# Optimization experiments

Measured on AMD Instinct MI355X. Metric: run time of the kernel, lower is better.

Reference implementation:

```python
import jax, jax.numpy as jnp
import numpy as np

H_S = 4
W_S = 4


def setup_inputs() -> dict:
    key = jax.random.key(0)
    k1, k2 = jax.random.split(key)
    x1 = jax.random.normal(k1, (8, 128, 96, 320), dtype=jnp.float32)
    x2 = jax.random.normal(k2, (8, 128, 96, 320), dtype=jnp.float32)
    return {"x1": x1, "x2": x2}


def reference(x1, x2):
    # torch F.pad p2d=(h_s,h_s,w_s,w_s) pads last dim (W) by h_s and H by w_s
    b, c, h, w = x1.shape
    padded = jnp.pad(x2, ((0, 0), (0, 0), (W_S, W_S), (H_S, H_S)))
    costs = []
    for y in range(2 * H_S + 1):
        for x in range(2 * W_S + 1):
            sl = padded[:, :, y:y + h, x:x + w]  # [B,C,H,W]
            costs.append(jnp.mean(x1 * sl, axis=1))  # [B,H,W]
    cost_vol = jnp.stack(costs, axis=1)  # [B,81,H,W]
    return jax.nn.leaky_relu(cost_vol, negative_slope=0.1)
```

## Files before the change

### kernel.cpp

```cpp
#include <hip/hip_runtime.h>
#include <stdint.h>


#define CCH   128
#define HH    96
#define WW    320
#define HWs   (HH * WW)
#define CHWs  (CCH * HWs)
#define ND    81

#define TH 4
#define WT 32
#define SW 40
#define SR 12
#define KC 32
#define KP 40
#define OP 132

typedef __attribute__((ext_vector_type(8))) short        short8;
typedef __attribute__((ext_vector_type(4))) float        floatx4;
typedef __attribute__((ext_vector_type(4))) unsigned int uint4v;

__device__ __forceinline__ unsigned int bf16rne(float f) {
  unsigned int u = __float_as_uint(f);
  return (u + 0x7fffu + ((u >> 16) & 1u)) >> 16;
}
__device__ __forceinline__ unsigned int pk2(float lo, float hi) {
  return bf16rne(lo) | (bf16rne(hi) << 16);
}

__global__ __launch_bounds__(512, 4) void cost_volume_kernel(
    const float* __restrict__ x1g, const float* __restrict__ x2g,
    float* __restrict__ out)
{
  extern __shared__ char smem[];
  short* x2s  = (short*)smem;
  float* obuf = (float*)smem;

  const int b  = blockIdx.x & 7;
  const int g  = blockIdx.x >> 3;
  const int hs = g % 24;
  const int ws = g / 24;
  const int h0 = hs * TH;
  const int W0 = ws * WT;

  const int t    = threadIdx.x;
  const int wave = t >> 6;
  const int lane = t & 63;
  const int hl   = wave >> 1;
  const int mt   = wave & 1;
  const int q    = lane >> 4;
  const int ln   = lane & 15;

  const float* x1b = x1g + (size_t)b * CHWs;
  const float* x2b = x2g + (size_t)b * CHWs;

  int x2_go[4], x2_lo[4];
#pragma unroll
  for (int s = 0; s < 4; ++s) {
    int u = t + s * 512;
    if (u < SR * SW * 4) {
      int j  = u % SW;
      int ro = u / SW;
      int o  = ro & 3;
      int r  = ro >> 2;
      int gr = h0 - 4 + r;
      int gc = W0 - 4 + j;
      x2_lo[s] = (r * SW + j) * KP + o * 8;
      x2_go[s] = (gr >= 0 && gr < HH && gc >= 0 && gc < WW)
                   ? (o * 8 * HWs + gr * WW + gc) : -1;
    } else { x2_lo[s] = -1; x2_go[s] = -1; }
  }
  const int x1off = (h0 + hl) * WW + W0 + mt * 16 + ln;

  floatx4 acc[9][2] = {};

  for (int kc = 0; kc < CCH / KC; ++kc) {
    const int cbase = kc * KC * HWs;

    const float* p1 = x1b + cbase + (size_t)q * 8 * HWs + x1off;
    float a0 = p1[0 * HWs], a1 = p1[1 * HWs], a2 = p1[2 * HWs], a3 = p1[3 * HWs];
    float a4 = p1[4 * HWs], a5 = p1[5 * HWs], a6 = p1[6 * HWs], a7 = p1[7 * HWs];

#pragma unroll
    for (int s = 0; s < 4; ++s) {
      if (x2_lo[s] >= 0) {
        unsigned int p01 = 0, p23 = 0, p45 = 0, p67 = 0;
        if (x2_go[s] >= 0) {
          const float* p = x2b + cbase + x2_go[s];
          float f0 = p[0 * HWs], f1 = p[1 * HWs], f2 = p[2 * HWs], f3 = p[3 * HWs];
          float f4 = p[4 * HWs], f5 = p[5 * HWs], f6 = p[6 * HWs], f7 = p[7 * HWs];
          p01 = pk2(f0, f1); p23 = pk2(f2, f3);
          p45 = pk2(f4, f5); p67 = pk2(f6, f7);
        }
        *(uint4v*)&x2s[x2_lo[s]] = (uint4v){p01, p23, p45, p67};
      }
    }

    short8 af;
    {
      uint4v av = (uint4v){pk2(a0, a1), pk2(a2, a3), pk2(a4, a5), pk2(a6, a7)};
      af = *(short8*)&av;
    }
    __syncthreads();

#pragma unroll
    for (int dyi = 0; dyi < 9; ++dyi) {
      const int r = hl + dyi;
#pragma unroll
      for (int jn = 0; jn < 2; ++jn) {
        int jc = (mt + jn) * 16 + ln;
        if (jc > SW - 1) jc = SW - 1;
        const short8 bf = *(const short8*)&x2s[(r * SW + jc) * KP + q * 8];
        acc[dyi][jn] = __builtin_amdgcn_mfma_f32_16x16x32_bf16(af, bf, acc[dyi][jn], 0, 0, 0);
      }
    }
    __syncthreads();
  }

  const size_t obase = (size_t)b * (ND * (size_t)HWs);
#pragma unroll
  for (int ph = 0; ph < 2; ++ph) {
    const int d0 = ph ? 5 : 0, d1 = ph ? 9 : 5;
#pragma unroll
    for (int dyi = 0; dyi < 9; ++dyi) {
      if (dyi < d0 || dyi >= d1) continue;
#pragma unroll
      for (int jn = 0; jn < 2; ++jn)
#pragma unroll
        for (int reg = 0; reg < 4; ++reg) {
          const int m   = q * 4 + reg;
          const int dxi = jn * 16 + ln - m;
          if (dxi >= 0 && dxi < 9) {
            float v = acc[dyi][jn][reg] * (1.0f / 128.0f);
            v = (v < 0.0f) ? 0.1f * v : v;
            obuf[((dyi - d0) * 9 + dxi) * OP + hl * WT + mt * 16 + m] = v;
          }
        }
    }
    __syncthreads();
    const int nd   = (d1 - d0) * 9;
    const int dbas = d0 * 9;
    for (int idx = t; idx < nd * TH * WT; idx += 512) {
      const int dl  = idx >> 7;
      const int rem = idx & 127;
      const int hh  = rem >> 5;
      const int wl  = rem & 31;
      out[obase + (size_t)(dbas + dl) * HWs + (h0 + hh) * WW + W0 + wl]
          = obuf[dl * OP + rem];
    }
    __syncthreads();
  }
}

extern "C" void kernel_launch(void* const* d_in, const int* in_sizes, int n_in,
                              void* d_out, int out_size, void* d_ws, size_t ws_size,
                              hipStream_t stream) {
  const float* x1 = (const float*)d_in[0];
  const float* x2 = (const float*)d_in[1];
  float* out = (float*)d_out;
  cost_volume_kernel<<<dim3(1920), dim3(512), 38400, stream>>>(x1, x2, out);
}
```

Before: 358.3 us.

## Double-buffer x2 LDS tile and prefetch next channel chunk into registers

The kernel now keeps two LDS buffers for the packed bf16 x2 tile. It issues the global loads for the next channel chunk before running the MFMA loop on the current one, then packs them into the other buffer afterwards, so each iteration needs one lightweight barrier instead of two __syncthreads. The aim is to hide global-load latency behind the matrix work. It also replaces the manual bf16 rounding with a native __bf16 conversion and lowers the launch-bounds occupancy hint from 4 to 3. Doubling dynamic LDS to 76.8 KB and keeping the prefetched data in registers may reduce how many blocks fit on each CU.

```diff
diff --git a/kernel.cpp b/kernel.cpp
--- a/kernel.cpp
+++ b/kernel.cpp
@@ -16,20 +16,25 @@
 #define KC 32
 #define KP 40
 #define OP 132
+#define BUFSH 19200
 
 typedef __attribute__((ext_vector_type(8))) short        short8;
 typedef __attribute__((ext_vector_type(4))) float        floatx4;
 typedef __attribute__((ext_vector_type(4))) unsigned int uint4v;
 
-__device__ __forceinline__ unsigned int bf16rne(float f) {
-  unsigned int u = __float_as_uint(f);
-  return (u + 0x7fffu + ((u >> 16) & 1u)) >> 16;
-}
 __device__ __forceinline__ unsigned int pk2(float lo, float hi) {
-  return bf16rne(lo) | (bf16rne(hi) << 16);
+  unsigned short a = __builtin_bit_cast(unsigned short, (__bf16)lo);
+  unsigned short b = __builtin_bit_cast(unsigned short, (__bf16)hi);
+  return (unsigned int)a | ((unsigned int)b << 16);
 }
 
-__global__ __launch_bounds__(512, 4) void cost_volume_kernel(
+__device__ __forceinline__ void pipe_barrier() {
+  asm volatile("s_waitcnt lgkmcnt(0)" ::: "memory");
+  __builtin_amdgcn_s_barrier();
+  asm volatile("" ::: "memory");
+}
+
+__global__ __launch_bounds__(512, 3) void cost_volume_kernel(
     const float* __restrict__ x1g, const float* __restrict__ x2g,
     float* __restrict__ out)
 {
@@ -73,37 +78,51 @@
   }
   const int x1off = (h0 + hl) * WW + W0 + mt * 16 + ln;
 
+  float xr[4][8];
+  float xa[8];
+  short8 af;
+
+  auto issue = [&](int kc) {
+    const int cbase = kc * KC * HWs;
+    const float* p1 = x1b + cbase + q * 8 * HWs + x1off;
+#pragma unroll
+    for (int i = 0; i < 8; ++i) xa[i] = p1[i * HWs];
+#pragma unroll
+    for (int s = 0; s < 4; ++s)
+      if (x2_go[s] >= 0) {
+        const float* p = x2b + cbase + x2_go[s];
+#pragma unroll
+        for (int i = 0; i < 8; ++i) xr[s][i] = p[i * HWs];
+      }
+  };
+
+  auto packw = [&](int kc) {
+    short* dst = x2s + (kc & 1) * BUFSH;
+#pragma unroll
+    for (int s = 0; s < 4; ++s)
+      if (x2_lo[s] >= 0) {
+        uint4v v = (uint4v){0u, 0u, 0u, 0u};
+        if (x2_go[s] >= 0)
+          v = (uint4v){pk2(xr[s][0], xr[s][1]), pk2(xr[s][2], xr[s][3]),
+                       pk2(xr[s][4], xr[s][5]), pk2(xr[s][6], xr[s][7])};
+        *(uint4v*)&dst[x2_lo[s]] = v;
+      }
+    uint4v av = (uint4v){pk2(xa[0], xa[1]), pk2(xa[2], xa[3]),
+                         pk2(xa[4], xa[5]), pk2(xa[6], xa[7])};
+    af = *(short8*)&av;
+  };
+
   floatx4 acc[9][2] = {};
 
-  for (int kc = 0; kc < CCH / KC; ++kc) {
-    const int cbase = kc * KC * HWs;
-
-    const float* p1 = x1b + cbase + (size_t)q * 8 * HWs + x1off;
-    float a0 = p1[0 * HWs], a1 = p1[1 * HWs], a2 = p1[2 * HWs], a3 = p1[3 * HWs];
-    float a4 = p1[4 * HWs], a5 = p1[5 * HWs], a6 = p1[6 * HWs], a7 = p1[7 * HWs];
+  issue(0);
+  packw(0);
 
 #pragma unroll
-    for (int s = 0; s < 4; ++s) {
-      if (x2_lo[s] >= 0) {
-        unsigned int p01 = 0, p23 = 0, p45 = 0, p67 = 0;
-        if (x2_go[s] >= 0) {
-          const float* p = x2b + cbase + x2_go[s];
-          float f0 = p[0 * HWs], f1 = p[1 * HWs], f2 = p[2 * HWs], f3 = p[3 * HWs];
-          float f4 = p[4 * HWs], f5 = p[5 * HWs], f6 = p[6 * HWs], f7 = p[7 * HWs];
-          p01 = pk2(f0, f1); p23 = pk2(f2, f3);
-          p45 = pk2(f4, f5); p67 = pk2(f6, f7);
-        }
-        *(uint4v*)&x2s[x2_lo[s]] = (uint4v){p01, p23, p45, p67};
-      }
-    }
-
-    short8 af;
-    {
-      uint4v av = (uint4v){pk2(a0, a1), pk2(a2, a3), pk2(a4, a5), pk2(a6, a7)};
-      af = *(short8*)&av;
-    }
-    __syncthreads();
-
+  for (int kc = 0; kc < CCH / KC; ++kc) {
+    if (kc < CCH / KC - 1) issue(kc + 1);
+    pipe_barrier();
+    const short* src = x2s + (kc & 1) * BUFSH;
+    const short8 a_cur = af;
 #pragma unroll
     for (int dyi = 0; dyi < 9; ++dyi) {
       const int r = hl + dyi;
@@ -111,11 +130,11 @@
       for (int jn = 0; jn < 2; ++jn) {
         int jc = (mt + jn) * 16 + ln;
         if (jc > SW - 1) jc = SW - 1;
-        const short8 bf = *(const short8*)&x2s[(r * SW + jc) * KP + q * 8];
-        acc[dyi][jn] = __builtin_amdgcn_mfma_f32_16x16x32_bf16(af, bf, acc[dyi][jn], 0, 0, 0);
+        const short8 bf = *(const short8*)&src[(r * SW + jc) * KP + q * 8];
+        acc[dyi][jn] = __builtin_amdgcn_mfma_f32_16x16x32_bf16(a_cur, bf, acc[dyi][jn], 0, 0, 0);
       }
     }
-    __syncthreads();
+    if (kc < CCH / KC - 1) packw(kc + 1);
   }
 
   const size_t obase = (size_t)b * (ND * (size_t)HWs);
@@ -159,5 +178,5 @@
   const float* x1 = (const float*)d_in[0];
   const float* x2 = (const float*)d_in[1];
   float* out = (float*)d_out;
-  cost_volume_kernel<<<dim3(1920), dim3(512), 38400, stream>>>(x1, x2, out);
+  cost_volume_kernel<<<dim3(1920), dim3(512), 2 * 38400, stream>>>(x1, x2, out);
 }
```

Result: slower. 384.9 us (+7.4%).

## Pre-pack x2 to swizzled bf16 workspace and double-buffer via global_load_lds DMA

Applied to the files above, without the earlier changes.

Adds a prepass kernel that converts x2 to bf16 once per launch into a channel-interleaved, slot-swizzled workspace layout, plus a shared zero page for out-of-bounds halo reads. The main kernel then streams those tiles straight into LDS with global_load_lds, double-buffered across channel chunks, and prefetches x1 for the next chunk while the MFMAs run. The aim is to remove the redundant fp32 loads and bf16 conversions of overlapping halo data in every block and to hide load latency. In exchange it costs an extra kernel launch, a workspace round trip of x2 through HBM, and more LDS per block (60 KB versus 38 KB), which may reduce occupancy.

```diff
diff --git a/kernel.cpp b/kernel.cpp
--- a/kernel.cpp
+++ b/kernel.cpp
@@ -14,22 +14,191 @@
 #define SW 40
 #define SR 12
 #define KC 32
-#define KP 40
 #define OP 132
+
+#define BUFB       30720
+#define X2WS_BYTES (8u*4u*96u*320u*64u)
+#define ZPAGE_OFF  X2WS_BYTES
+#define WS_NEED    (X2WS_BYTES + 4096u)
+#define CHUNK_STEP (96*320*64)
 
 typedef __attribute__((ext_vector_type(8))) short        short8;
 typedef __attribute__((ext_vector_type(4))) float        floatx4;
 typedef __attribute__((ext_vector_type(4))) unsigned int uint4v;
 
-__device__ __forceinline__ unsigned int bf16rne(float f) {
-  unsigned int u = __float_as_uint(f);
-  return (u + 0x7fffu + ((u >> 16) & 1u)) >> 16;
-}
 __device__ __forceinline__ unsigned int pk2(float lo, float hi) {
-  return bf16rne(lo) | (bf16rne(hi) << 16);
-}
-
-__global__ __launch_bounds__(512, 4) void cost_volume_kernel(
+  unsigned short a = __builtin_bit_cast(unsigned short, (__bf16)lo);
+  unsigned short b = __builtin_bit_cast(unsigned short, (__bf16)hi);
+  return (unsigned int)a | ((unsigned int)b << 16);
+}
+
+#define GLOAD_LDS16(gp, lp) __builtin_amdgcn_global_load_lds(              \
+    (const __attribute__((address_space(1))) void*)(gp),                   \
+    (__attribute__((address_space(3))) void*)(lp), 16, 0, 0)
+
+__global__ __launch_bounds__(320) void x2_prepass(
+    const float* __restrict__ x2g, char* __restrict__ ws)
+{
+  const int idx = blockIdx.x;
+  const int h  = idx % 96;
+  const int kc = (idx / 96) & 3;
+  const int b  = idx / 384;
+  const int gc = threadIdx.x;
+
+  const float* src = x2g + (size_t)b * CHWs + (size_t)(kc * 32) * HWs
+                   + h * WW + gc;
+  float v[32];
+#pragma unroll
+  for (int c = 0; c < 32; ++c) v[c] = src[c * HWs];
+
+  char* dst = ws + ((size_t)((b * 4 + kc) * 96 + h) * 320 + gc) * 64;
+  const int hgc = ((gc + 4) >> 1) & 3;
+#pragma unroll
+  for (int q = 0; q < 4; ++q) {
+    uint4v w = (uint4v){pk2(v[8*q+0], v[8*q+1]), pk2(v[8*q+2], v[8*q+3]),
+                        pk2(v[8*q+4], v[8*q+5]), pk2(v[8*q+6], v[8*q+7])};
+    const int s = (q + hgc) & 3;
+    *(uint4v*)(dst + s * 16) = w;
+  }
+
+  if (idx == 0 && threadIdx.x < 256)
+    *(uint4v*)(ws + ZPAGE_OFF + threadIdx.x * 16) = (uint4v){0u, 0u, 0u, 0u};
+}
+
+__global__ __launch_bounds__(512, 4) void cost_volume_main(
+    const float* __restrict__ x1g, const char* __restrict__ ws2,
+    float* __restrict__ out)
+{
+  extern __shared__ char smem[];
+  short* x2s  = (short*)smem;
+  float* obuf = (float*)smem;
+
+  const int b  = blockIdx.x & 7;
+  const int g  = blockIdx.x >> 3;
+  const int hs = g % 24;
+  const int wsx = g / 24;
+  const int h0 = hs * TH;
+  const int W0 = wsx * WT;
+
+  const int t    = threadIdx.x;
+  const int wave = t >> 6;
+  const int lane = t & 63;
+  const int hl   = wave >> 1;
+  const int mt   = wave & 1;
+  const int q    = lane >> 4;
+  const int ln   = lane & 15;
+
+  unsigned int off[4];
+  unsigned int vm = 0;
+#pragma unroll
+  for (int si = 0; si < 4; ++si) {
+    const int iid = wave * 4 + si;
+    if (iid < 30) {
+      const int unit = iid * 64 + lane;
+      const int r  = unit / 160;
+      const int rem = unit - r * 160;
+      const int j  = rem >> 2;
+      const int s  = rem & 3;
+      const int gr = h0 - 4 + r;
+      const int gc = W0 - 4 + j;
+      const bool inb = (gr >= 0 && gr < HH && gc >= 0 && gc < WW);
+      off[si] = inb ? (unsigned)(((b * 4) * HH + gr) * WW + gc) * 64u + s * 16u
+                    : (unsigned)(ZPAGE_OFF + s * 16u);
+      if (inb) vm |= (1u << si);
+    } else off[si] = ZPAGE_OFF;
+  }
+
+  const float* x1b  = x1g + (size_t)b * CHWs;
+  const int    x1off = (h0 + hl) * WW + W0 + mt * 16 + ln;
+
+  auto issue_dma = [&](int kc1) {
+    char* lb = smem + (kc1 & 1) * BUFB + wave * 4096;
+#pragma unroll
+    for (int si = 0; si < 4; ++si) {
+      if (wave * 4 + si < 30) {
+        GLOAD_LDS16(ws2 + off[si], lb + si * 1024);
+        off[si] += (vm >> si & 1u) ? (unsigned)CHUNK_STEP : 0u;
+      }
+    }
+  };
+
+  float xa[8];
+  auto issue_x1 = [&](int kc1) {
+    const float* p1 = x1b + kc1 * KC * HWs + q * 8 * HWs + x1off;
+#pragma unroll
+    for (int i = 0; i < 8; ++i) xa[i] = p1[i * HWs];
+  };
+
+  floatx4 acc[9][2] = {};
+
+  issue_dma(0);
+  issue_x1(0);
+
+#pragma unroll
+  for (int kc = 0; kc < CCH / KC; ++kc) {
+    uint4v av = (uint4v){pk2(xa[0], xa[1]), pk2(xa[2], xa[3]),
+                         pk2(xa[4], xa[5]), pk2(xa[6], xa[7])};
+    const short8 af = *(short8*)&av;
+    asm volatile("s_waitcnt vmcnt(0)" ::: "memory");
+    __builtin_amdgcn_s_barrier();
+    asm volatile("" ::: "memory");
+
+    if (kc < CCH / KC - 1) { issue_dma(kc + 1); issue_x1(kc + 1); }
+
+    const short* src = x2s + (kc & 1) * (BUFB / 2);
+    __builtin_amdgcn_s_setprio(1);
+#pragma unroll
+    for (int dyi = 0; dyi < 9; ++dyi) {
+      const int r = hl + dyi;
+#pragma unroll
+      for (int jn = 0; jn < 2; ++jn) {
+        int j = (mt + jn) * 16 + ln;
+        if (j > SW - 1) j = SW - 1;
+        const int slot = (q + (j >> 1)) & 3;
+        const short8 bf = *(const short8*)&src[((r * SW + j) * 4 + slot) * 8];
+        acc[dyi][jn] = __builtin_amdgcn_mfma_f32_16x16x32_bf16(af, bf, acc[dyi][jn], 0, 0, 0);
+      }
+    }
+    __builtin_amdgcn_s_setprio(0);
+  }
+
+  const size_t obase = (size_t)b * (ND * (size_t)HWs);
+#pragma unroll
+  for (int ph = 0; ph < 2; ++ph) {
+    const int d0 = ph ? 5 : 0, d1 = ph ? 9 : 5;
+#pragma unroll
+    for (int dyi = 0; dyi < 9; ++dyi) {
+      if (dyi < d0 || dyi >= d1) continue;
+#pragma unroll
+      for (int jn = 0; jn < 2; ++jn)
+#pragma unroll
+        for (int reg = 0; reg < 4; ++reg) {
+          const int m   = q * 4 + reg;
+          const int dxi = jn * 16 + ln - m;
+          if (dxi >= 0 && dxi < 9) {
+            float v = acc[dyi][jn][reg] * (1.0f / 128.0f);
+            v = (v < 0.0f) ? 0.1f * v : v;
+            obuf[((dyi - d0) * 9 + dxi) * OP + hl * WT + mt * 16 + m] = v;
+          }
+        }
+    }
+    __syncthreads();
+    const int nd   = (d1 - d0) * 9;
+    const int dbas = d0 * 9;
+    for (int idx = t; idx < nd * TH * WT; idx += 512) {
+      const int dl  = idx >> 7;
+      const int rem = idx & 127;
+      const int hh  = rem >> 5;
+      const int wl  = rem & 31;
+      out[obase + (size_t)(dbas + dl) * HWs + (h0 + hh) * WW + W0 + wl]
+          = obuf[dl * OP + rem];
+    }
+    __syncthreads();
+  }
+}
+
+#define KP 40
+__global__ __launch_bounds__(512, 4) void cost_volume_fallback(
     const float* __restrict__ x1g, const float* __restrict__ x2g,
     float* __restrict__ out)
 {
@@ -40,9 +209,9 @@
   const int b  = blockIdx.x & 7;
   const int g  = blockIdx.x >> 3;
   const int hs = g % 24;
-  const int ws = g / 24;
+  const int wsx = g / 24;
   const int h0 = hs * TH;
-  const int W0 = ws * WT;
+  const int W0 = wsx * WT;
 
   const int t    = threadIdx.x;
   const int wave = t >> 6;
@@ -77,7 +246,6 @@
 
   for (int kc = 0; kc < CCH / KC; ++kc) {
     const int cbase = kc * KC * HWs;
-
     const float* p1 = x1b + cbase + (size_t)q * 8 * HWs + x1off;
     float a0 = p1[0 * HWs], a1 = p1[1 * HWs], a2 = p1[2 * HWs], a3 = p1[3 * HWs];
     float a4 = p1[4 * HWs], a5 = p1[5 * HWs], a6 = p1[6 * HWs], a7 = p1[7 * HWs];
@@ -159,5 +327,11 @@
   const float* x1 = (const float*)d_in[0];
   const float* x2 = (const float*)d_in[1];
   float* out = (float*)d_out;
-  cost_volume_kernel<<<dim3(1920), dim3(512), 38400, stream>>>(x1, x2, out);
-}
+  if (ws_size >= (size_t)WS_NEED && d_ws != nullptr) {
+    x2_prepass<<<dim3(8 * 4 * 96), dim3(320), 0, stream>>>(x2, (char*)d_ws);
+    cost_volume_main<<<dim3(1920), dim3(512), 2 * BUFB, stream>>>(
+        x1, (const char*)d_ws, out);
+  } else {
+    cost_volume_fallback<<<dim3(1920), dim3(512), 38400, stream>>>(x1, x2, out);
+  }
+}
```

Result: faster. 317.7 us (-11.3%).
